# Performance work log

Measured on AMD Instinct MI355X. Metric: run time of the kernel, lower is better.

Reference implementation:

```python
import jax, jax.numpy as jnp
import numpy as np

B, I, O, G = 4096, 256, 256, 16


def setup_inputs() -> dict:
    key = jax.random.key(0)
    k1, k2 = jax.random.split(key)
    x = jax.random.normal(k1, (B, I), dtype=jnp.float32)
    # xavier_uniform bound for fan_in=I*G (last dim), fan_out=O treated per torch default on 4D: use small scale
    bound = float(np.sqrt(6.0 / (I * G + O * G)))
    laplacecoeffs = jax.random.uniform(k2, (2, O, I, G), dtype=jnp.float32, minval=-bound, maxval=bound)
    bias = jnp.zeros((1, O), dtype=jnp.float32)
    return {"x": x, "laplacecoeffs": laplacecoeffs, "bias": bias}


def reference(x, laplacecoeffs, bias):
    # x: (B, I); laplacecoeffs: (2, O, I, G); bias: (1, O)
    g = laplacecoeffs.shape[-1]  # static gridsize (clamped/rounded gridsize_param at init)
    lambdas = jnp.linspace(0.1, 1.0, g).astype(x.dtype)  # (G,)
    e = x[:, :, None] * lambdas  # (B, I, G)
    exp_neg = jnp.exp(-e)
    exp_pos = jnp.exp(e)
    # contract over (inputdim, gridsize) without materializing (B, O, I, G)
    y = jnp.einsum('big,oig->bo', exp_neg, laplacecoeffs[0])
    y = y + jnp.einsum('big,oig->bo', exp_pos, laplacecoeffs[1])
    y = y + bias  # (B, O)
    return y
```

## Files before the change

### kernel.cpp

```cpp
#include <hip/hip_runtime.h>


typedef __bf16 bf16x8 __attribute__((ext_vector_type(8)));
typedef __bf16 bf16x4 __attribute__((ext_vector_type(4)));
typedef float  f32x4  __attribute__((ext_vector_type(4)));

#define M_TOT 4096
#define N_TOT 256
#define MN_TOT (M_TOT * N_TOT)
#define SPLITK 8

__device__ __forceinline__ void gload_lds16(const __bf16* g, __bf16* l) {
  __builtin_amdgcn_global_load_lds(
      (const __attribute__((address_space(1))) void*)g,
      (__attribute__((address_space(3))) void*)l, 16, 0, 0);
}

__global__ void convert_w(const float* __restrict__ C, __bf16* __restrict__ W) {
  int t = blockIdx.x * 256 + threadIdx.x;
  int E = t << 2;
  int c = E >> 12, x4 = E & 4095;
  int s = c >> 8, o = c & 255;
  const f32x4 v = *(const f32x4*)(C + (size_t)c * 4096 + x4);
  bf16x4 w;
  w[0] = (__bf16)v[0]; w[1] = (__bf16)v[1]; w[2] = (__bf16)v[2]; w[3] = (__bf16)v[3];
  *(bf16x4*)(W + (size_t)o * 8192 + (size_t)s * 4096 + x4) = w;
}

template <int MODE>
__global__ __launch_bounds__(256, 4)
void laplace_gemm(const float* __restrict__ X, const __bf16* __restrict__ Wb,
                  const float* __restrict__ Bias, float* __restrict__ Out,
                  float* __restrict__ P) {
  __shared__ __bf16 As[64 * 72];
  __shared__ __bf16 Bs[128 * 64];

  const int tid = threadIdx.x;
  const int mt = blockIdx.x, nt = blockIdx.y, kt = blockIdx.z;
  const int m0 = mt * 64, n0 = nt * 128;
  const int s   = kt >> 2;
  const int i0c = (kt & 3) * 64;

  const int wv = tid >> 6, lane = tid & 63;
  const int wm = wv & 1, wn = wv >> 1;
  const int lm = lane & 15, q = lane >> 4;

  const int mr0 = tid >> 2, ii0 = tid & 3;
  const float* xp0 = X + (size_t)(m0 + mr0) * 256 + i0c + ii0;

  const float sgn = s ? 1.0f : -1.0f;
  const float c0 = 0.1f * sgn, cd = 0.06f * sgn;

  const f32x4 zero = {0.f, 0.f, 0.f, 0.f};
  f32x4 acc[2][4];
#pragma unroll
  for (int a = 0; a < 2; ++a)
#pragma unroll
    for (int b = 0; b < 4; ++b) acc[a][b] = zero;

  const size_t wrow = (size_t)s * 4096 + (size_t)i0c * 16;

  float xc0 = *xp0;

  for (int j = 0; j < 16; ++j) {
    const size_t kw = wrow + (size_t)j * 64;
#pragma unroll
    for (int qq = 0; qq < 4; ++qq) {
      const int idx = qq * 256 + tid;
      const int r = idx >> 3, cc = idx & 7;
      const __bf16* gsrc = Wb + (size_t)(n0 + r) * 8192 + kw + ((cc ^ (r & 7)) << 3);
      __bf16* ldst = Bs + ((qq * 256 + (tid & ~63)) << 3);
      gload_lds16(gsrc, ldst);
    }

    float xn0 = 0.f;
    if (j < 15) xn0 = xp0[4 * (j + 1)];

    {
      const float p = __expf(c0 * xc0), r = __expf(cd * xc0);
      const float r2 = r * r, r4 = r2 * r2, r8 = r4 * r4;
      bf16x8 v0, v1; float f = p, f2 = p * r8;
#pragma unroll
      for (int h = 0; h < 8; ++h) { v0[h] = (__bf16)f;  f  *= r; }
#pragma unroll
      for (int h = 0; h < 8; ++h) { v1[h] = (__bf16)f2; f2 *= r; }
      *(bf16x8*)&As[mr0 * 72 + ii0 * 16]     = v0;
      *(bf16x8*)&As[mr0 * 72 + ii0 * 16 + 8] = v1;
    }

    __syncthreads();

#pragma unroll
    for (int kk = 0; kk < 2; ++kk) {
      bf16x8 af[2], bfr[4];
#pragma unroll
      for (int a = 0; a < 2; ++a)
        af[a] = *(const bf16x8*)&As[(wm * 32 + a * 16 + lm) * 72 + kk * 32 + q * 8];
      const int pc8 = (((kk << 2) + q) ^ (lm & 7)) << 3;
#pragma unroll
      for (int b = 0; b < 4; ++b)
        bfr[b] = *(const bf16x8*)&Bs[(wn * 64 + b * 16 + lm) * 64 + pc8];
#pragma unroll
      for (int a = 0; a < 2; ++a)
#pragma unroll
        for (int b = 0; b < 4; ++b)
          acc[a][b] = __builtin_amdgcn_mfma_f32_16x16x32_bf16(af[a], bfr[b], acc[a][b], 0, 0, 0);
    }
    __syncthreads();

    xc0 = xn0;
  }

  if constexpr (MODE == 0) {
    float* Pk = P + (size_t)kt * MN_TOT;
#pragma unroll
    for (int a = 0; a < 2; ++a) {
      const int mrow = m0 + wm * 32 + a * 16 + q * 4;
#pragma unroll
      for (int rr = 0; rr < 4; ++rr)
#pragma unroll
        for (int b = 0; b < 4; ++b) {
          const int n = n0 + wn * 64 + b * 16 + lm;
          Pk[(size_t)(mrow + rr) * 256 + n] = acc[a][b][rr];
        }
    }
  } else {
#pragma unroll
    for (int a = 0; a < 2; ++a) {
      const int mrow = m0 + wm * 32 + a * 16 + q * 4;
#pragma unroll
      for (int rr = 0; rr < 4; ++rr)
#pragma unroll
        for (int b = 0; b < 4; ++b) {
          const int n = n0 + wn * 64 + b * 16 + lm;
          float v = acc[a][b][rr];
          if (kt == 0) v += Bias[n];
          atomicAdd(&Out[(size_t)(mrow + rr) * 256 + n], v);
        }
    }
  }
}

__global__ void reduce_bias(const float* __restrict__ P, const float* __restrict__ Bias,
                            float* __restrict__ Out) {
  const int t = blockIdx.x * 256 + threadIdx.x;
  const size_t base = (size_t)t * 4;
  f32x4 sv = *(const f32x4*)&P[base];
#pragma unroll
  for (int k = 1; k < SPLITK; ++k) sv += *(const f32x4*)&P[(size_t)k * MN_TOT + base];
  sv += *(const f32x4*)&Bias[base & 255];
  *(f32x4*)&Out[base] = sv;
}

extern "C" void kernel_launch(void* const* d_in, const int* in_sizes, int n_in,
                              void* d_out, int out_size, void* d_ws, size_t ws_size,
                              hipStream_t stream) {
  const float* X    = (const float*)d_in[0];
  const float* C    = (const float*)d_in[1];
  const float* Bias = (const float*)d_in[2];
  float* Out = (float*)d_out;

  __bf16* Wb = (__bf16*)d_ws;
  const size_t wb_bytes = (size_t)N_TOT * 8192 * sizeof(__bf16);
  const size_t p_bytes  = (size_t)SPLITK * MN_TOT * sizeof(float);
  float* P = (float*)((char*)d_ws + wb_bytes);

  convert_w<<<2048, 256, 0, stream>>>(C, Wb);

  if (ws_size >= wb_bytes + p_bytes) {
    laplace_gemm<0><<<dim3(64, 2, SPLITK), 256, 0, stream>>>(X, Wb, Bias, Out, P);
    reduce_bias<<<1024, 256, 0, stream>>>(P, Bias, Out);
  } else {
    hipMemsetAsync(d_out, 0, (size_t)out_size * sizeof(float), stream);
    laplace_gemm<1><<<dim3(64, 2, SPLITK), 256, 0, stream>>>(X, Wb, Bias, Out, P);
  }
}
```

Baseline: 93.73 us.

## Drop split-K partials and reduction; use smaller tiles with full-K loop

```diff
diff --git a/kernel.cpp b/kernel.cpp
--- a/kernel.cpp
+++ b/kernel.cpp
@@ -7,8 +7,6 @@
 
 #define M_TOT 4096
 #define N_TOT 256
-#define MN_TOT (M_TOT * N_TOT)
-#define SPLITK 8
 
 __device__ __forceinline__ void gload_lds16(const __bf16* g, __bf16* l) {
   __builtin_amdgcn_global_load_lds(
@@ -27,129 +25,82 @@
   *(bf16x4*)(W + (size_t)o * 8192 + (size_t)s * 4096 + x4) = w;
 }
 
-template <int MODE>
 __global__ __launch_bounds__(256, 4)
 void laplace_gemm(const float* __restrict__ X, const __bf16* __restrict__ Wb,
-                  const float* __restrict__ Bias, float* __restrict__ Out,
-                  float* __restrict__ P) {
-  __shared__ __bf16 As[64 * 72];
-  __shared__ __bf16 Bs[128 * 64];
+                  const float* __restrict__ Bias, float* __restrict__ Out) {
+  __shared__ __bf16 Bs[64 * 128];
+  __shared__ __bf16 As[32 * 136];
 
   const int tid = threadIdx.x;
-  const int mt = blockIdx.x, nt = blockIdx.y, kt = blockIdx.z;
-  const int m0 = mt * 64, n0 = nt * 128;
-  const int s   = kt >> 2;
-  const int i0c = (kt & 3) * 64;
+  const int m0 = blockIdx.x * 32, n0 = blockIdx.y * 64;
 
   const int wv = tid >> 6, lane = tid & 63;
   const int wm = wv & 1, wn = wv >> 1;
   const int lm = lane & 15, q = lane >> 4;
 
-  const int mr0 = tid >> 2, ii0 = tid & 3;
-  const float* xp0 = X + (size_t)(m0 + mr0) * 256 + i0c + ii0;
-
-  const float sgn = s ? 1.0f : -1.0f;
-  const float c0 = 0.1f * sgn, cd = 0.06f * sgn;
+  const int row = tid >> 3, di = tid & 7;
+  const float* xrowp = X + (size_t)(m0 + row) * 256 + di;
 
   const f32x4 zero = {0.f, 0.f, 0.f, 0.f};
-  f32x4 acc[2][4];
-#pragma unroll
-  for (int a = 0; a < 2; ++a)
-#pragma unroll
-    for (int b = 0; b < 4; ++b) acc[a][b] = zero;
+  f32x4 acc[2] = {zero, zero};
 
-  const size_t wrow = (size_t)s * 4096 + (size_t)i0c * 16;
+  float xc = xrowp[0];
 
-  float xc0 = *xp0;
+  for (int j = 0; j < 64; ++j) {
+    const int jj = j & 31, s = j >> 5;
+    const size_t kb = (size_t)s * 4096 + (size_t)jj * 128;
 
-  for (int j = 0; j < 16; ++j) {
-    const size_t kw = wrow + (size_t)j * 64;
 #pragma unroll
     for (int qq = 0; qq < 4; ++qq) {
       const int idx = qq * 256 + tid;
-      const int r = idx >> 3, cc = idx & 7;
-      const __bf16* gsrc = Wb + (size_t)(n0 + r) * 8192 + kw + ((cc ^ (r & 7)) << 3);
+      const int r = idx >> 4, cc = idx & 15;
+      const __bf16* gsrc = Wb + (size_t)(n0 + r) * 8192 + kb + ((cc ^ (r & 15)) << 3);
       __bf16* ldst = Bs + ((qq * 256 + (tid & ~63)) << 3);
       gload_lds16(gsrc, ldst);
     }
 
-    float xn0 = 0.f;
-    if (j < 15) xn0 = xp0[4 * (j + 1)];
+    float xn = 0.f;
+    if (j < 63) xn = xrowp[((j + 1) & 31) * 8];
 
     {
-      const float p = __expf(c0 * xc0), r = __expf(cd * xc0);
+      const float sgn = s ? 1.0f : -1.0f;
+      const float p = __expf(0.1f * sgn * xc), r = __expf(0.06f * sgn * xc);
       const float r2 = r * r, r4 = r2 * r2, r8 = r4 * r4;
       bf16x8 v0, v1; float f = p, f2 = p * r8;
 #pragma unroll
       for (int h = 0; h < 8; ++h) { v0[h] = (__bf16)f;  f  *= r; }
 #pragma unroll
       for (int h = 0; h < 8; ++h) { v1[h] = (__bf16)f2; f2 *= r; }
-      *(bf16x8*)&As[mr0 * 72 + ii0 * 16]     = v0;
-      *(bf16x8*)&As[mr0 * 72 + ii0 * 16 + 8] = v1;
+      *(bf16x8*)&As[row * 136 + di * 16]     = v0;
+      *(bf16x8*)&As[row * 136 + di * 16 + 8] = v1;
     }
 
     __syncthreads();
 
 #pragma unroll
-    for (int kk = 0; kk < 2; ++kk) {
-      bf16x8 af[2], bfr[4];
+    for (int kk = 0; kk < 4; ++kk) {
+      bf16x8 af = *(const bf16x8*)&As[(wm * 16 + lm) * 136 + kk * 32 + q * 8];
+      const int pc = ((kk << 2) + q) ^ lm;
 #pragma unroll
-      for (int a = 0; a < 2; ++a)
-        af[a] = *(const bf16x8*)&As[(wm * 32 + a * 16 + lm) * 72 + kk * 32 + q * 8];
-      const int pc8 = (((kk << 2) + q) ^ (lm & 7)) << 3;
-#pragma unroll
-      for (int b = 0; b < 4; ++b)
-        bfr[b] = *(const bf16x8*)&Bs[(wn * 64 + b * 16 + lm) * 64 + pc8];
-#pragma unroll
-      for (int a = 0; a < 2; ++a)
-#pragma unroll
-        for (int b = 0; b < 4; ++b)
-          acc[a][b] = __builtin_amdgcn_mfma_f32_16x16x32_bf16(af[a], bfr[b], acc[a][b], 0, 0, 0);
+      for (int b = 0; b < 2; ++b) {
+        bf16x8 bfr = *(const bf16x8*)&Bs[(wn * 32 + b * 16 + lm) * 128 + (pc << 3)];
+        acc[b] = __builtin_amdgcn_mfma_f32_16x16x32_bf16(af, bfr, acc[b], 0, 0, 0);
+      }
     }
     __syncthreads();
 
-    xc0 = xn0;
+    xc = xn;
   }
 
-  if constexpr (MODE == 0) {
-    float* Pk = P + (size_t)kt * MN_TOT;
 #pragma unroll
-    for (int a = 0; a < 2; ++a) {
-      const int mrow = m0 + wm * 32 + a * 16 + q * 4;
+  for (int b = 0; b < 2; ++b) {
+    const int n = n0 + wn * 32 + b * 16 + lm;
+    const float bias = Bias[n];
+    const int mrow = m0 + wm * 16 + q * 4;
 #pragma unroll
-      for (int rr = 0; rr < 4; ++rr)
-#pragma unroll
-        for (int b = 0; b < 4; ++b) {
-          const int n = n0 + wn * 64 + b * 16 + lm;
-          Pk[(size_t)(mrow + rr) * 256 + n] = acc[a][b][rr];
-        }
-    }
-  } else {
-#pragma unroll
-    for (int a = 0; a < 2; ++a) {
-      const int mrow = m0 + wm * 32 + a * 16 + q * 4;
-#pragma unroll
-      for (int rr = 0; rr < 4; ++rr)
-#pragma unroll
-        for (int b = 0; b < 4; ++b) {
-          const int n = n0 + wn * 64 + b * 16 + lm;
-          float v = acc[a][b][rr];
-          if (kt == 0) v += Bias[n];
-          atomicAdd(&Out[(size_t)(mrow + rr) * 256 + n], v);
-        }
-    }
+    for (int rr = 0; rr < 4; ++rr)
+      Out[(size_t)(mrow + rr) * 256 + n] = acc[b][rr] + bias;
   }
-}
-
-__global__ void reduce_bias(const float* __restrict__ P, const float* __restrict__ Bias,
-                            float* __restrict__ Out) {
-  const int t = blockIdx.x * 256 + threadIdx.x;
-  const size_t base = (size_t)t * 4;
-  f32x4 sv = *(const f32x4*)&P[base];
-#pragma unroll
-  for (int k = 1; k < SPLITK; ++k) sv += *(const f32x4*)&P[(size_t)k * MN_TOT + base];
-  sv += *(const f32x4*)&Bias[base & 255];
-  *(f32x4*)&Out[base] = sv;
 }
 
 extern "C" void kernel_launch(void* const* d_in, const int* in_sizes, int n_in,
@@ -161,17 +112,7 @@
   float* Out = (float*)d_out;
 
   __bf16* Wb = (__bf16*)d_ws;
-  const size_t wb_bytes = (size_t)N_TOT * 8192 * sizeof(__bf16);
-  const size_t p_bytes  = (size_t)SPLITK * MN_TOT * sizeof(float);
-  float* P = (float*)((char*)d_ws + wb_bytes);
 
   convert_w<<<2048, 256, 0, stream>>>(C, Wb);
-
-  if (ws_size >= wb_bytes + p_bytes) {
-    laplace_gemm<0><<<dim3(64, 2, SPLITK), 256, 0, stream>>>(X, Wb, Bias, Out, P);
-    reduce_bias<<<1024, 256, 0, stream>>>(P, Bias, Out);
-  } else {
-    hipMemsetAsync(d_out, 0, (size_t)out_size * sizeof(float), stream);
-    laplace_gemm<1><<<dim3(64, 2, SPLITK), 256, 0, stream>>>(X, Wb, Bias, Out, P);
-  }
+  laplace_gemm<<<dim3(128, 4), 256, 0, stream>>>(X, Wb, Bias, Out);
 }
```

After: 126.6 us. 1.35x slower.

## Drop LDS staging; load MFMA operands directly into registers with double buffering

Applied to the files above, without the earlier changes.

```diff
diff --git a/kernel.cpp b/kernel.cpp
--- a/kernel.cpp
+++ b/kernel.cpp
@@ -9,12 +9,6 @@
 #define N_TOT 256
 #define MN_TOT (M_TOT * N_TOT)
 #define SPLITK 8
-
-__device__ __forceinline__ void gload_lds16(const __bf16* g, __bf16* l) {
-  __builtin_amdgcn_global_load_lds(
-      (const __attribute__((address_space(1))) void*)g,
-      (__attribute__((address_space(3))) void*)l, 16, 0, 0);
-}
 
 __global__ void convert_w(const float* __restrict__ C, __bf16* __restrict__ W) {
   int t = blockIdx.x * 256 + threadIdx.x;
@@ -28,116 +22,97 @@
 }
 
 template <int MODE>
-__global__ __launch_bounds__(256, 4)
+__global__ __launch_bounds__(128, 1)
 void laplace_gemm(const float* __restrict__ X, const __bf16* __restrict__ Wb,
                   const float* __restrict__ Bias, float* __restrict__ Out,
                   float* __restrict__ P) {
-  __shared__ __bf16 As[64 * 72];
-  __shared__ __bf16 Bs[128 * 64];
-
   const int tid = threadIdx.x;
-  const int mt = blockIdx.x, nt = blockIdx.y, kt = blockIdx.z;
-  const int m0 = mt * 64, n0 = nt * 128;
-  const int s   = kt >> 2;
-  const int i0c = (kt & 3) * 64;
-
-  const int wv = tid >> 6, lane = tid & 63;
-  const int wm = wv & 1, wn = wv >> 1;
+  const int mt = blockIdx.x, ks = blockIdx.y;
+  const int w = tid >> 6, lane = tid & 63;
   const int lm = lane & 15, q = lane >> 4;
 
-  const int mr0 = tid >> 2, ii0 = tid & 3;
-  const float* xp0 = X + (size_t)(m0 + mr0) * 256 + i0c + ii0;
-
+  const int s = ks >> 2;
+  const int ibase = (ks & 3) * 64 + (q >> 1);
   const float sgn = s ? 1.0f : -1.0f;
   const float c0 = 0.1f * sgn, cd = 0.06f * sgn;
+  const bool qodd = (q & 1) != 0;
+
+  const float* xr0 = X + (size_t)(mt * 64 +  0 + lm) * 256 + ibase;
+  const float* xr1 = X + (size_t)(mt * 64 + 16 + lm) * 256 + ibase;
+  const float* xr2 = X + (size_t)(mt * 64 + 32 + lm) * 256 + ibase;
+  const float* xr3 = X + (size_t)(mt * 64 + 48 + lm) * 256 + ibase;
+
+  const __bf16* bb = Wb + (size_t)(w * 128 + lm) * 8192 + ks * 1024 + q * 8;
 
   const f32x4 zero = {0.f, 0.f, 0.f, 0.f};
-  f32x4 acc[2][4];
+  f32x4 acc[4][8];
 #pragma unroll
-  for (int a = 0; a < 2; ++a)
+  for (int a = 0; a < 4; ++a)
 #pragma unroll
-    for (int b = 0; b < 4; ++b) acc[a][b] = zero;
+    for (int b = 0; b < 8; ++b) acc[a][b] = zero;
 
-  const size_t wrow = (size_t)s * 4096 + (size_t)i0c * 16;
+  bf16x8 Bf[2][8];
+  float  xv[2][4];
 
-  float xc0 = *xp0;
+#pragma unroll
+  for (int b = 0; b < 8; ++b)
+    Bf[0][b] = *(const bf16x8*)(bb + (size_t)b * 131072);
+  xv[0][0] = xr0[0]; xv[0][1] = xr1[0]; xv[0][2] = xr2[0]; xv[0][3] = xr3[0];
 
-  for (int j = 0; j < 16; ++j) {
-    const size_t kw = wrow + (size_t)j * 64;
+#pragma unroll 2
+  for (int j = 0; j < 32; ++j) {
+    const int cur = j & 1, nxt = cur ^ 1;
+    const int jn = (j < 31) ? (j + 1) : 0;
+
 #pragma unroll
-    for (int qq = 0; qq < 4; ++qq) {
-      const int idx = qq * 256 + tid;
-      const int r = idx >> 3, cc = idx & 7;
-      const __bf16* gsrc = Wb + (size_t)(n0 + r) * 8192 + kw + ((cc ^ (r & 7)) << 3);
-      __bf16* ldst = Bs + ((qq * 256 + (tid & ~63)) << 3);
-      gload_lds16(gsrc, ldst);
+    for (int b = 0; b < 8; ++b)
+      Bf[nxt][b] = *(const bf16x8*)(bb + (size_t)b * 131072 + jn * 32);
+    xv[nxt][0] = xr0[2 * jn]; xv[nxt][1] = xr1[2 * jn];
+    xv[nxt][2] = xr2[2 * jn]; xv[nxt][3] = xr3[2 * jn];
+
+    bf16x8 Af[4];
+#pragma unroll
+    for (int a = 0; a < 4; ++a) {
+      const float x = xv[cur][a];
+      const float p = __expf(c0 * x), r = __expf(cd * x);
+      const float r2 = r * r, r4 = r2 * r2, r8 = r4 * r4;
+      float f = qodd ? p * r8 : p;
+#pragma unroll
+      for (int h = 0; h < 8; ++h) { Af[a][h] = (__bf16)f; f *= r; }
     }
 
-    float xn0 = 0.f;
-    if (j < 15) xn0 = xp0[4 * (j + 1)];
-
-    {
-      const float p = __expf(c0 * xc0), r = __expf(cd * xc0);
-      const float r2 = r * r, r4 = r2 * r2, r8 = r4 * r4;
-      bf16x8 v0, v1; float f = p, f2 = p * r8;
 #pragma unroll
-      for (int h = 0; h < 8; ++h) { v0[h] = (__bf16)f;  f  *= r; }
+    for (int a = 0; a < 4; ++a)
 #pragma unroll
-      for (int h = 0; h < 8; ++h) { v1[h] = (__bf16)f2; f2 *= r; }
-      *(bf16x8*)&As[mr0 * 72 + ii0 * 16]     = v0;
-      *(bf16x8*)&As[mr0 * 72 + ii0 * 16 + 8] = v1;
-    }
-
-    __syncthreads();
-
-#pragma unroll
-    for (int kk = 0; kk < 2; ++kk) {
-      bf16x8 af[2], bfr[4];
-#pragma unroll
-      for (int a = 0; a < 2; ++a)
-        af[a] = *(const bf16x8*)&As[(wm * 32 + a * 16 + lm) * 72 + kk * 32 + q * 8];
-      const int pc8 = (((kk << 2) + q) ^ (lm & 7)) << 3;
-#pragma unroll
-      for (int b = 0; b < 4; ++b)
-        bfr[b] = *(const bf16x8*)&Bs[(wn * 64 + b * 16 + lm) * 64 + pc8];
-#pragma unroll
-      for (int a = 0; a < 2; ++a)
-#pragma unroll
-        for (int b = 0; b < 4; ++b)
-          acc[a][b] = __builtin_amdgcn_mfma_f32_16x16x32_bf16(af[a], bfr[b], acc[a][b], 0, 0, 0);
-    }
-    __syncthreads();
-
-    xc0 = xn0;
+      for (int b = 0; b < 8; ++b)
+        acc[a][b] = __builtin_amdgcn_mfma_f32_16x16x32_bf16(Af[a], Bf[cur][b], acc[a][b], 0, 0, 0);
   }
 
   if constexpr (MODE == 0) {
-    float* Pk = P + (size_t)kt * MN_TOT;
+    float* Pk = P + (size_t)ks * MN_TOT + (size_t)w * 128;
 #pragma unroll
-    for (int a = 0; a < 2; ++a) {
-      const int mrow = m0 + wm * 32 + a * 16 + q * 4;
+    for (int a = 0; a < 4; ++a)
 #pragma unroll
-      for (int rr = 0; rr < 4; ++rr)
+      for (int rr = 0; rr < 4; ++rr) {
+        const int mrow = mt * 64 + a * 16 + q * 4 + rr;
 #pragma unroll
-        for (int b = 0; b < 4; ++b) {
-          const int n = n0 + wn * 64 + b * 16 + lm;
-          Pk[(size_t)(mrow + rr) * 256 + n] = acc[a][b][rr];
-        }
-    }
+        for (int b = 0; b < 8; ++b)
+          Pk[(size_t)mrow * 256 + b * 16 + lm] = acc[a][b][rr];
+      }
   } else {
 #pragma unroll
-    for (int a = 0; a < 2; ++a) {
-      const int mrow = m0 + wm * 32 + a * 16 + q * 4;
+    for (int a = 0; a < 4; ++a)
 #pragma unroll
-      for (int rr = 0; rr < 4; ++rr)
+      for (int rr = 0; rr < 4; ++rr) {
+        const int mrow = mt * 64 + a * 16 + q * 4 + rr;
 #pragma unroll
-        for (int b = 0; b < 4; ++b) {
-          const int n = n0 + wn * 64 + b * 16 + lm;
+        for (int b = 0; b < 8; ++b) {
+          const int n = w * 128 + b * 16 + lm;
           float v = acc[a][b][rr];
-          if (kt == 0) v += Bias[n];
-          atomicAdd(&Out[(size_t)(mrow + rr) * 256 + n], v);
+          if (ks == 0) v += Bias[n];
+          atomicAdd(&Out[(size_t)mrow * 256 + n], v);
         }
-    }
+      }
   }
 }
 
@@ -168,10 +143,10 @@
   convert_w<<<2048, 256, 0, stream>>>(C, Wb);
 
   if (ws_size >= wb_bytes + p_bytes) {
-    laplace_gemm<0><<<dim3(64, 2, SPLITK), 256, 0, stream>>>(X, Wb, Bias, Out, P);
+    laplace_gemm<0><<<dim3(64, SPLITK), 128, 0, stream>>>(X, Wb, Bias, Out, P);
     reduce_bias<<<1024, 256, 0, stream>>>(P, Bias, Out);
   } else {
     hipMemsetAsync(d_out, 0, (size_t)out_size * sizeof(float), stream);
-    laplace_gemm<1><<<dim3(64, 2, SPLITK), 256, 0, stream>>>(X, Wb, Bias, Out, P);
+    laplace_gemm<1><<<dim3(64, SPLITK), 128, 0, stream>>>(X, Wb, Bias, Out, P);
   }
 }
```

After: 118.9 us. +26.9%, slower.
